# Performance work log

Hardware: AMD Instinct MI355X
Metric: run time of the kernel (lower is better)

## Reference

```python
import jax, jax.numpy as jnp
import numpy as np


def _bipolarize(x):
    # torchhd.hard_quantize: sign quantize to {-1, +1}
    return jnp.where(x > 0, 1.0, -1.0).astype(x.dtype)


def _transform(am, projections):
    """PQ-HDC Algorithm 1: MAP AM (C,D) -> binary AM (C,P,D) in {0,1} + weights (C,P)."""
    C, D = am.shape

    def per_class(hv):  # hv: (D,)
        bips = []
        loss = hv
        for _ in range(projections):  # P is small (2-4), sequential by construction
            bip = _bipolarize(loss)
            dot = jnp.dot(loss, bip)
            # orthogonal projection of loss onto bip: bip * dot / ||bip||^2
            loss = loss - bip * dot / jnp.sum(bip * bip)
            bips.append(bip)
        X = jnp.stack(bips)  # (P, D) bipolar
        G = X @ X.T  # (P, P)
        w = hv @ X.T @ jnp.linalg.inv(G)  # (P,)
        # normalize: length of w[:,None]*X over full (P,D) matrix
        length = jnp.linalg.norm(w[:, None] * X)
        w = jnp.sqrt(jnp.asarray(D, hv.dtype)) * w / length
        w = w ** 2
        return X, w

    Xs, ws = jax.vmap(per_class)(am)  # (C,P,D), (C,P)
    ambin = jnp.where(Xs > 0, 1.0, 0.0).astype(am.dtype)  # binarize {0,1}
    return ambin, ws


def _phs(qbin, ambin, weights):
    """Pseudo Hamming Similarity, batched. qbin:(B,D) {0,1}; ambin:(C,P,D) {0,1}."""
    D = qbin.shape[-1]
    # equal-bit count = D - sum(q XOR a) = D - sum_q - sum_a + 2*q.a
    dots = jnp.einsum('bd,cpd->bcp', qbin, ambin)  # (B,C,P)
    qsum = jnp.sum(qbin, axis=-1)                  # (B,)
    asum = jnp.sum(ambin, axis=-1)                 # (C,P)
    ham = D - qsum[:, None, None] - asum[None, :, :] + 2.0 * dots
    return jnp.sum(weights[None, :, :] * ham, axis=-1)  # (B,C)


def setup_inputs() -> dict:
    key = jax.random.key(0)
    k1, k2 = jax.random.split(key)
    B, C, D = 4096, 128, 10000
    query = jax.random.normal(k1, (B, D), dtype=jnp.float32)
    am = jax.random.normal(k2, (C, D), dtype=jnp.float32)
    return {"query": query, "am": am, "projections": 3}


def reference(query, am, projections):
    ambin, weights = _transform(am, projections)
    qbin = jnp.where(_bipolarize(query) > 0, 1.0, 0.0).astype(query.dtype)
    return _phs(qbin, ambin, weights)  # (B, C) logits
```

## Files before the change

### kernel.cpp

```cpp
#include <hip/hip_runtime.h>
#include <stdint.h>

typedef unsigned long long u64;
typedef __attribute__((ext_vector_type(4))) unsigned int u32x4;

#define D_DIM   10000
#define C_CLS   128
#define WPRP    192
#define NWORDS  160
#define NIT     40
#define GRP     8

__device__ __forceinline__ float wred64(float v) {
#pragma unroll
    for (int m = 1; m <= 32; m <<= 1) v += __shfl_xor(v, m);
    return v;
}
__device__ __forceinline__ int wred64i(int v) {
#pragma unroll
    for (int m = 1; m <= 32; m <<= 1) v += __shfl_xor(v, m);
    return v;
}

__device__ __forceinline__ size_t am_idx(int c, int wi, int p) {
    return ((size_t)c * 32 + (unsigned)wi / 6u) * 18 + (size_t)p * 6 + (unsigned)wi % 6u;
}

__global__ __launch_bounds__(256) void kA_transform(const float* __restrict__ am,
                                                    u64* __restrict__ amw,
                                                    float4* __restrict__ wtab)
{
    const int c = blockIdx.x;
    const int t = threadIdx.x;
    const int w = t >> 6;
    const int l = t & 63;

    __shared__ float redf[4];
    __shared__ int   sI[4][6];
    __shared__ float sF[4][3];

    const float* hvp = am + (size_t)c * D_DIM;

    float4 loss[10], hv[10];
#pragma unroll
    for (int k = 0; k < 10; ++k) {
        const int it = w + 4 * k;
        const int d0 = it * 256 + 4 * l;
        float4 x = make_float4(0.f, 0.f, 0.f, 0.f);
        if (d0 + 3 < D_DIM) x = *(const float4*)(hvp + d0);
        loss[k] = x; hv[k] = x;
    }

    int cnt[3]; float hX[3]; u64 sp[3];

#pragma unroll
    for (int p = 0; p < 3; ++p) {
        float sabs = 0.f;
#pragma unroll
        for (int k = 0; k < 10; ++k)
            sabs += fabsf(loss[k].x) + fabsf(loss[k].y) + fabsf(loss[k].z) + fabsf(loss[k].w);
        sabs = wred64(sabs);
        if (l == 0) redf[w] = sabs;
        __syncthreads();
        const float dot = redf[0] + redf[1] + redf[2] + redf[3];
        __syncthreads();
        const float dd = dot / (float)D_DIM;

        u64 bits = 0; int cc = 0; float hx = 0.f;
#pragma unroll
        for (int k = 0; k < 10; ++k) {
            const int it = w + 4 * k;
            const bool p0 = loss[k].x > 0.f;
            const bool p1 = loss[k].y > 0.f;
            const bool p2 = loss[k].z > 0.f;
            const bool p3 = loss[k].w > 0.f;
            const u64 b0 = __ballot(p0);
            const u64 b1 = __ballot(p1);
            const u64 b2 = __ballot(p2);
            const u64 b3 = __ballot(p3);
            if (l < 4) {
                const u64 bb = (l == 0) ? b0 : ((l == 1) ? b1 : ((l == 2) ? b2 : b3));
                amw[am_idx(c, it * 4 + l, p)] = bb;
            }
            bits |= ((u64)p0 << (4 * k)) | ((u64)p1 << (4 * k + 1))
                  | ((u64)p2 << (4 * k + 2)) | ((u64)p3 << (4 * k + 3));
            cc += (int)p0 + (int)p1 + (int)p2 + (int)p3;
            hx += (p0 ? hv[k].x : -hv[k].x) + (p1 ? hv[k].y : -hv[k].y)
                + (p2 ? hv[k].z : -hv[k].z) + (p3 ? hv[k].w : -hv[k].w);
            float4 L = loss[k];
            L.x -= p0 ? dd : -dd; L.y -= p1 ? dd : -dd;
            L.z -= p2 ? dd : -dd; L.w -= p3 ? dd : -dd;
            const int d0 = it * 256 + 4 * l;
            if (!(d0 + 3 < D_DIM)) L = make_float4(0.f, 0.f, 0.f, 0.f);
            loss[k] = L;
        }
        if (t < WPRP - NWORDS) amw[am_idx(c, NWORDS + t, p)] = 0ull;
        sp[p] = bits; cnt[p] = cc; hX[p] = hx;
    }

    int vi[6] = { cnt[0], cnt[1], cnt[2],
                  static_cast<int>(__popcll(sp[0] ^ sp[1])),
                  static_cast<int>(__popcll(sp[0] ^ sp[2])),
                  static_cast<int>(__popcll(sp[1] ^ sp[2])) };
#pragma unroll
    for (int i = 0; i < 6; ++i) vi[i] = wred64i(vi[i]);
    float vf[3] = { hX[0], hX[1], hX[2] };
#pragma unroll
    for (int i = 0; i < 3; ++i) vf[i] = wred64(vf[i]);
    if (l == 0) {
#pragma unroll
        for (int i = 0; i < 6; ++i) sI[w][i] = vi[i];
#pragma unroll
        for (int i = 0; i < 3; ++i) sF[w][i] = vf[i];
    }
    __syncthreads();
    if (t == 0) {
        int a0 = 0, a1 = 0, a2 = 0, X01 = 0, X02 = 0, X12 = 0;
        float h0f = 0, h1f = 0, h2f = 0;
        for (int i = 0; i < 4; ++i) {
            a0 += sI[i][0]; a1 += sI[i][1]; a2 += sI[i][2];
            X01 += sI[i][3]; X02 += sI[i][4]; X12 += sI[i][5];
            h0f += sF[i][0]; h1f += sF[i][1]; h2f += sF[i][2];
        }
        const double Dv = (double)D_DIM;
        const double h0 = h0f, h1 = h1f, h2 = h2f;
        const double g01 = Dv - 2.0 * X01, g02 = Dv - 2.0 * X02, g12 = Dv - 2.0 * X12;
        const double A00 = Dv * Dv - g12 * g12;
        const double A01 = g02 * g12 - g01 * Dv;
        const double A02 = g01 * g12 - g02 * Dv;
        const double A11 = Dv * Dv - g02 * g02;
        const double A12 = g02 * g01 - Dv * g12;
        const double A22 = Dv * Dv - g01 * g01;
        const double det = Dv * A00 + g01 * A01 + g02 * A02;
        const double w0 = (A00 * h0 + A01 * h1 + A02 * h2) / det;
        const double w1 = (A01 * h0 + A11 * h1 + A12 * h2) / det;
        const double w2 = (A02 * h0 + A12 * h1 + A22 * h2) / det;
        const double s = w0 * w0 + w1 * w1 + w2 * w2;
        const double f0 = w0 * w0 / s, f1 = w1 * w1 / s, f2 = w2 * w2 / s;
        const double cb = -(f0 * a0 + f1 * a1 + f2 * a2);
        wtab[c] = make_float4((float)f0, (float)f1, (float)f2, (float)cb);
    }
}

struct AmBatch { u32x4 r[9]; };

__device__ __forceinline__ void amload_asm(AmBatch& b, const u64* ap) {
    asm("global_load_dwordx4 %0, %9, off\n\t"
        "global_load_dwordx4 %1, %9, off offset:16\n\t"
        "global_load_dwordx4 %2, %9, off offset:32\n\t"
        "global_load_dwordx4 %3, %9, off offset:48\n\t"
        "global_load_dwordx4 %4, %9, off offset:64\n\t"
        "global_load_dwordx4 %5, %9, off offset:80\n\t"
        "global_load_dwordx4 %6, %9, off offset:96\n\t"
        "global_load_dwordx4 %7, %9, off offset:112\n\t"
        "global_load_dwordx4 %8, %9, off offset:128\n\t"
        "s_waitcnt vmcnt(0)"
        : "=v"(b.r[0]), "=v"(b.r[1]), "=v"(b.r[2]), "=v"(b.r[3]), "=v"(b.r[4]),
          "=v"(b.r[5]), "=v"(b.r[6]), "=v"(b.r[7]), "=v"(b.r[8])
        : "v"(ap));
}

__device__ __forceinline__ void qload4_asm(float4& x0, float4& x1, float4& x2, float4& x3,
                                           const float* p) {
    asm("global_load_dwordx4 %0, %4, off\n\t"
        "global_load_dwordx4 %1, %4, off offset:1024\n\t"
        "global_load_dwordx4 %2, %4, off offset:2048\n\t"
        "global_load_dwordx4 %3, %4, off offset:3072\n\t"
        "s_waitcnt vmcnt(0)"
        : "=v"(x0), "=v"(x1), "=v"(x2), "=v"(x3)
        : "v"(p));
}

__global__ __launch_bounds__(256, 4) void kB_phs(const float* __restrict__ query,
                                                 const u64* __restrict__ amw,
                                                 const float4* __restrict__ wtab,
                                                 float* __restrict__ out)
{
    __shared__ u64 qlds[4 * WPRP];
    __shared__ float4 wsh[C_CLS];
    __shared__ float part[4][4][GRP][33];
    const int t = threadIdx.x;
    const int w = t >> 6;
    const int l = t & 63;
    const int r0 = blockIdx.x * 4;
    const int wl = l & 31;
    const int c0 = 32 * w;

    if (t < C_CLS) wsh[t] = wtab[t];

    {
        const float* qp = query + (size_t)(r0 + w) * D_DIM;
        u64* qrow = qlds + w * WPRP;
        for (int ib = 0; ib < 9; ++ib) {
            const int it0 = ib * 4;
            float4 x0, x1, x2, x3;
            qload4_asm(x0, x1, x2, x3, qp + it0 * 256 + 4 * l);
            float4 xs[4] = { x0, x1, x2, x3 };
#pragma unroll
            for (int k = 0; k < 4; ++k) {
                const u64 b0 = __ballot(xs[k].x > 0.f);
                const u64 b1 = __ballot(xs[k].y > 0.f);
                const u64 b2 = __ballot(xs[k].z > 0.f);
                const u64 b3 = __ballot(xs[k].w > 0.f);
                if (l < 4) qrow[(it0 + k) * 4 + l] =
                    (l == 0) ? b0 : ((l == 1) ? b1 : ((l == 2) ? b2 : b3));
            }
        }
        for (int it = 36; it < NIT; ++it) {
            const int d0 = it * 256 + 4 * l;
            float4 x = make_float4(0.f, 0.f, 0.f, 0.f);
            if (d0 + 3 < D_DIM) x = *(const float4*)(qp + d0);
            const u64 b0 = __ballot(x.x > 0.f);
            const u64 b1 = __ballot(x.y > 0.f);
            const u64 b2 = __ballot(x.z > 0.f);
            const u64 b3 = __ballot(x.w > 0.f);
            if (l < 4) qrow[it * 4 + l] = (l == 0) ? b0 : ((l == 1) ? b1 : ((l == 2) ? b2 : b3));
        }
        if (l < 32) qrow[NWORDS + l] = 0ull;
    }
    __syncthreads();

    const int rh = l >> 5;
    const int rA = 2 * rh, rB = 2 * rh + 1;

    const u64* qaP = qlds + rA * WPRP + wl * 6;
    const u64* qbP = qlds + rB * WPRP + wl * 6;
    unsigned qa32[12], qb32[12];
#pragma unroll
    for (int i = 0; i < 6; ++i) {
        const u64 a = qaP[i], b = qbP[i];
        qa32[2 * i] = (unsigned)a; qa32[2 * i + 1] = (unsigned)(a >> 32);
        qb32[2 * i] = (unsigned)b; qb32[2 * i + 1] = (unsigned)(b >> 32);
    }

    int qsA = 0, qsB = 0;
#pragma unroll
    for (int i = 0; i < 12; ++i) { qsA += __popc(qa32[i]); qsB += __popc(qb32[i]); }
    const float offA = 312.5f - (float)qsA;
    const float offB = 312.5f - (float)qsB;

    const int o = l >> 1;
    const int row_loc = o >> 3;
    const int cc = o & 7;
    const int h = l & 1;

    float (*pw)[GRP][33] = part[w];

    for (int g = 0; g < 4; ++g) {
        const int cbase = c0 + g * GRP;
        float accA[GRP], accB[GRP];
#pragma unroll
        for (int i = 0; i < GRP; ++i) {
            const int c = cbase + i;
            AmBatch b;
            amload_asm(b, amw + ((size_t)c * 32 + wl) * 18);
            int pA[3] = {0, 0, 0}, pB[3] = {0, 0, 0};
#pragma unroll
            for (int p = 0; p < 3; ++p)
#pragma unroll
                for (int k = 0; k < 3; ++k) {
                    const u32x4 v = b.r[3 * p + k];
                    pA[p] += __popc(qa32[4 * k + 0] & v[0]) + __popc(qa32[4 * k + 1] & v[1])
                           + __popc(qa32[4 * k + 2] & v[2]) + __popc(qa32[4 * k + 3] & v[3]);
                    pB[p] += __popc(qb32[4 * k + 0] & v[0]) + __popc(qb32[4 * k + 1] & v[1])
                           + __popc(qb32[4 * k + 2] & v[2]) + __popc(qb32[4 * k + 3] & v[3]);
                }
            const float4 wv = wsh[c];
            const float cw = wv.w * 0.03125f;
            accA[i] = fmaf(2.f, wv.x * (float)pA[0] + wv.y * (float)pA[1] + wv.z * (float)pA[2],
                           offA + cw);
            accB[i] = fmaf(2.f, wv.x * (float)pB[0] + wv.y * (float)pB[1] + wv.z * (float)pB[2],
                           offB + cw);
        }

#pragma unroll
        for (int i = 0; i < GRP; ++i) {
            pw[rA][i][wl] = accA[i];
            pw[rB][i][wl] = accB[i];
        }
        float s = 0.f;
#pragma unroll
        for (int j = 0; j < 16; ++j) s += pw[row_loc][cc][h * 16 + j];
        s += __shfl_xor(s, 1);
        if (h == 0)
            out[(size_t)(r0 + row_loc) * C_CLS + (cbase + cc)] = s;
    }
}

extern "C" void kernel_launch(void* const* d_in, const int* in_sizes, int n_in,
                              void* d_out, int out_size, void* d_ws, size_t ws_size,
                              hipStream_t stream)
{
    const float* query = (const float*)d_in[0];
    const float* am    = (const float*)d_in[1];
    float* out = (float*)d_out;

    float4* wtab = (float4*)d_ws;
    u64* amw = (u64*)((char*)d_ws + 2048);

    const int B = in_sizes[0] / D_DIM;

    hipLaunchKernelGGL(kA_transform, dim3(C_CLS), dim3(256), 0, stream, am, amw, wtab);
    hipLaunchKernelGGL(kB_phs, dim3(B / 4), dim3(256), 0, stream, query, amw, wtab, out);
}
```

Before: 97.24 us.

## Halve rows per block, split query binarization across waves, raise occupancy

Each block now handles 2 query rows instead of 4, and each lane holds one row's bits instead of two. The query sign-packing work is split so two waves cooperate on each row's word range. Launch bounds move to 8 blocks per SM and the reduction becomes a 4-lane shuffle. The inline-asm load outputs are marked early-clobber so the compiler cannot alias them with the address register. This doubles the number of blocks and the AM bit-vector reloads per query row, trading more global and L2 traffic on the AM table for lower register pressure and more parallelism.

```diff
diff --git a/kernel.cpp b/kernel.cpp
--- a/kernel.cpp
+++ b/kernel.cpp
@@ -155,8 +155,8 @@
         "global_load_dwordx4 %7, %9, off offset:112\n\t"
         "global_load_dwordx4 %8, %9, off offset:128\n\t"
         "s_waitcnt vmcnt(0)"
-        : "=v"(b.r[0]), "=v"(b.r[1]), "=v"(b.r[2]), "=v"(b.r[3]), "=v"(b.r[4]),
-          "=v"(b.r[5]), "=v"(b.r[6]), "=v"(b.r[7]), "=v"(b.r[8])
+        : "=&v"(b.r[0]), "=&v"(b.r[1]), "=&v"(b.r[2]), "=&v"(b.r[3]), "=&v"(b.r[4]),
+          "=&v"(b.r[5]), "=&v"(b.r[6]), "=&v"(b.r[7]), "=&v"(b.r[8])
         : "v"(ap));
 }
 
@@ -167,32 +167,36 @@
         "global_load_dwordx4 %2, %4, off offset:2048\n\t"
         "global_load_dwordx4 %3, %4, off offset:3072\n\t"
         "s_waitcnt vmcnt(0)"
-        : "=v"(x0), "=v"(x1), "=v"(x2), "=v"(x3)
+        : "=&v"(x0), "=&v"(x1), "=&v"(x2), "=&v"(x3)
         : "v"(p));
 }
 
-__global__ __launch_bounds__(256, 4) void kB_phs(const float* __restrict__ query,
+__global__ __launch_bounds__(256, 8) void kB_phs(const float* __restrict__ query,
                                                  const u64* __restrict__ amw,
                                                  const float4* __restrict__ wtab,
                                                  float* __restrict__ out)
 {
-    __shared__ u64 qlds[4 * WPRP];
+    __shared__ u64 qlds[2 * WPRP];
     __shared__ float4 wsh[C_CLS];
-    __shared__ float part[4][4][GRP][33];
+    __shared__ float part[4][2][GRP][33];
     const int t = threadIdx.x;
     const int w = t >> 6;
     const int l = t & 63;
-    const int r0 = blockIdx.x * 4;
+    const int r0 = blockIdx.x * 2;
     const int wl = l & 31;
     const int c0 = 32 * w;
 
     if (t < C_CLS) wsh[t] = wtab[t];
 
     {
-        const float* qp = query + (size_t)(r0 + w) * D_DIM;
-        u64* qrow = qlds + w * WPRP;
-        for (int ib = 0; ib < 9; ++ib) {
-            const int it0 = ib * 4;
+        const int row = w & 1;
+        const int half = w >> 1;
+        const float* qp = query + (size_t)(r0 + row) * D_DIM;
+        u64* qrow = qlds + row * WPRP;
+        const int itBase = 20 * half;
+        const int nb = (half == 0) ? 5 : 4;
+        for (int ib = 0; ib < nb; ++ib) {
+            const int it0 = itBase + ib * 4;
             float4 x0, x1, x2, x3;
             qload4_asm(x0, x1, x2, x3, qp + it0 * 256 + 4 * l);
             float4 xs[4] = { x0, x1, x2, x3 };
@@ -206,82 +210,72 @@
                     (l == 0) ? b0 : ((l == 1) ? b1 : ((l == 2) ? b2 : b3));
             }
         }
-        for (int it = 36; it < NIT; ++it) {
-            const int d0 = it * 256 + 4 * l;
-            float4 x = make_float4(0.f, 0.f, 0.f, 0.f);
-            if (d0 + 3 < D_DIM) x = *(const float4*)(qp + d0);
-            const u64 b0 = __ballot(x.x > 0.f);
-            const u64 b1 = __ballot(x.y > 0.f);
-            const u64 b2 = __ballot(x.z > 0.f);
-            const u64 b3 = __ballot(x.w > 0.f);
-            if (l < 4) qrow[it * 4 + l] = (l == 0) ? b0 : ((l == 1) ? b1 : ((l == 2) ? b2 : b3));
-        }
-        if (l < 32) qrow[NWORDS + l] = 0ull;
+        if (half == 1) {
+            for (int it = 36; it < NIT; ++it) {
+                const int d0 = it * 256 + 4 * l;
+                float4 x = make_float4(0.f, 0.f, 0.f, 0.f);
+                if (d0 + 3 < D_DIM) x = *(const float4*)(qp + d0);
+                const u64 b0 = __ballot(x.x > 0.f);
+                const u64 b1 = __ballot(x.y > 0.f);
+                const u64 b2 = __ballot(x.z > 0.f);
+                const u64 b3 = __ballot(x.w > 0.f);
+                if (l < 4) qrow[it * 4 + l] = (l == 0) ? b0 : ((l == 1) ? b1 : ((l == 2) ? b2 : b3));
+            }
+        }
+        if (w < 2 && l < 32) qlds[w * WPRP + NWORDS + l] = 0ull;
     }
     __syncthreads();
 
-    const int rh = l >> 5;
-    const int rA = 2 * rh, rB = 2 * rh + 1;
-
-    const u64* qaP = qlds + rA * WPRP + wl * 6;
-    const u64* qbP = qlds + rB * WPRP + wl * 6;
-    unsigned qa32[12], qb32[12];
+    const int rowh = l >> 5;
+    const u64* qP = qlds + rowh * WPRP + wl * 6;
+    unsigned q32[12];
 #pragma unroll
     for (int i = 0; i < 6; ++i) {
-        const u64 a = qaP[i], b = qbP[i];
-        qa32[2 * i] = (unsigned)a; qa32[2 * i + 1] = (unsigned)(a >> 32);
-        qb32[2 * i] = (unsigned)b; qb32[2 * i + 1] = (unsigned)(b >> 32);
-    }
-
-    int qsA = 0, qsB = 0;
-#pragma unroll
-    for (int i = 0; i < 12; ++i) { qsA += __popc(qa32[i]); qsB += __popc(qb32[i]); }
-    const float offA = 312.5f - (float)qsA;
-    const float offB = 312.5f - (float)qsB;
-
-    const int o = l >> 1;
+        const u64 a = qP[i];
+        q32[2 * i] = (unsigned)a; q32[2 * i + 1] = (unsigned)(a >> 32);
+    }
+    int qs = 0;
+#pragma unroll
+    for (int i = 0; i < 12; ++i) qs += __popc(q32[i]);
+    const float off = 312.5f - (float)qs;
+
+    const int o = l >> 2;
     const int row_loc = o >> 3;
     const int cc = o & 7;
-    const int h = l & 1;
+    const int h = l & 3;
 
     float (*pw)[GRP][33] = part[w];
 
     for (int g = 0; g < 4; ++g) {
         const int cbase = c0 + g * GRP;
-        float accA[GRP], accB[GRP];
+        float acc[GRP];
 #pragma unroll
         for (int i = 0; i < GRP; ++i) {
             const int c = cbase + i;
             AmBatch b;
             amload_asm(b, amw + ((size_t)c * 32 + wl) * 18);
-            int pA[3] = {0, 0, 0}, pB[3] = {0, 0, 0};
+            int pc[3] = {0, 0, 0};
 #pragma unroll
             for (int p = 0; p < 3; ++p)
 #pragma unroll
                 for (int k = 0; k < 3; ++k) {
                     const u32x4 v = b.r[3 * p + k];
-                    pA[p] += __popc(qa32[4 * k + 0] & v[0]) + __popc(qa32[4 * k + 1] & v[1])
-                           + __popc(qa32[4 * k + 2] & v[2]) + __popc(qa32[4 * k + 3] & v[3]);
-                    pB[p] += __popc(qb32[4 * k + 0] & v[0]) + __popc(qb32[4 * k + 1] & v[1])
-                           + __popc(qb32[4 * k + 2] & v[2]) + __popc(qb32[4 * k + 3] & v[3]);
+                    pc[p] += __popc(q32[4 * k + 0] & v[0]) + __popc(q32[4 * k + 1] & v[1])
+                           + __popc(q32[4 * k + 2] & v[2]) + __popc(q32[4 * k + 3] & v[3]);
                 }
             const float4 wv = wsh[c];
             const float cw = wv.w * 0.03125f;
-            accA[i] = fmaf(2.f, wv.x * (float)pA[0] + wv.y * (float)pA[1] + wv.z * (float)pA[2],
-                           offA + cw);
-            accB[i] = fmaf(2.f, wv.x * (float)pB[0] + wv.y * (float)pB[1] + wv.z * (float)pB[2],
-                           offB + cw);
-        }
-
-#pragma unroll
-        for (int i = 0; i < GRP; ++i) {
-            pw[rA][i][wl] = accA[i];
-            pw[rB][i][wl] = accB[i];
-        }
+            acc[i] = fmaf(2.f, wv.x * (float)pc[0] + wv.y * (float)pc[1] + wv.z * (float)pc[2],
+                          off + cw);
+        }
+
+#pragma unroll
+        for (int i = 0; i < GRP; ++i) pw[rowh][i][wl] = acc[i];
         float s = 0.f;
 #pragma unroll
-        for (int j = 0; j < 16; ++j) s += pw[row_loc][cc][h * 16 + j];
+        for (int j = 0; j < 8; ++j) s += pw[row_loc][cc][h * 8 + j];
         s += __shfl_xor(s, 1);
+        s += __shfl_xor(s, 2);
         if (h == 0)
             out[(size_t)(r0 + row_loc) * C_CLS + (cbase + cc)] = s;
     }
@@ -301,5 +295,5 @@
     const int B = in_sizes[0] / D_DIM;
 
     hipLaunchKernelGGL(kA_transform, dim3(C_CLS), dim3(256), 0, stream, am, amw, wtab);
-    hipLaunchKernelGGL(kB_phs, dim3(B / 4), dim3(256), 0, stream, query, amw, wtab, out);
-}
+    hipLaunchKernelGGL(kB_phs, dim3(B / 2), dim3(256), 0, stream, query, amw, wtab, out);
+}
```

Measured after the change: 170.7 us. 1.76x slower.

## Split query packing into separate kernel and double PHS grid over class halves

Applied to the files above, without the earlier changes.

Query bit-packing moves out of the PHS kernel into a standalone pack kernel that writes packed rows to workspace. The PHS kernel then reads packed query words from global memory and launches twice as many blocks, each covering half the classes, to raise parallelism. The inline asm load outputs also become early-clobber. The trade-off is an extra launch and a global round trip for the packed queries, and the old fused kernel is kept as a fallback when the workspace is too small.

```diff
diff --git a/kernel.cpp b/kernel.cpp
--- a/kernel.cpp
+++ b/kernel.cpp
@@ -155,8 +155,8 @@
         "global_load_dwordx4 %7, %9, off offset:112\n\t"
         "global_load_dwordx4 %8, %9, off offset:128\n\t"
         "s_waitcnt vmcnt(0)"
-        : "=v"(b.r[0]), "=v"(b.r[1]), "=v"(b.r[2]), "=v"(b.r[3]), "=v"(b.r[4]),
-          "=v"(b.r[5]), "=v"(b.r[6]), "=v"(b.r[7]), "=v"(b.r[8])
+        : "=&v"(b.r[0]), "=&v"(b.r[1]), "=&v"(b.r[2]), "=&v"(b.r[3]), "=&v"(b.r[4]),
+          "=&v"(b.r[5]), "=&v"(b.r[6]), "=&v"(b.r[7]), "=&v"(b.r[8])
         : "v"(ap));
 }
 
@@ -167,64 +167,71 @@
         "global_load_dwordx4 %2, %4, off offset:2048\n\t"
         "global_load_dwordx4 %3, %4, off offset:3072\n\t"
         "s_waitcnt vmcnt(0)"
-        : "=v"(x0), "=v"(x1), "=v"(x2), "=v"(x3)
+        : "=&v"(x0), "=&v"(x1), "=&v"(x2), "=&v"(x3)
         : "v"(p));
 }
 
-__global__ __launch_bounds__(256, 4) void kB_phs(const float* __restrict__ query,
-                                                 const u64* __restrict__ amw,
-                                                 const float4* __restrict__ wtab,
-                                                 float* __restrict__ out)
+__global__ __launch_bounds__(256, 4) void kB1_pack(const float* __restrict__ query,
+                                                   u64* __restrict__ qws)
 {
-    __shared__ u64 qlds[4 * WPRP];
+    const int t = threadIdx.x;
+    const int w = t >> 6;
+    const int l = t & 63;
+    const int row = blockIdx.x * 4 + w;
+
+    const float* qp = query + (size_t)row * D_DIM;
+    u64* qrow = qws + (size_t)row * WPRP;
+    for (int ib = 0; ib < 9; ++ib) {
+        const int it0 = ib * 4;
+        float4 x0, x1, x2, x3;
+        qload4_asm(x0, x1, x2, x3, qp + it0 * 256 + 4 * l);
+        float4 xs[4] = { x0, x1, x2, x3 };
+#pragma unroll
+        for (int k = 0; k < 4; ++k) {
+            const u64 b0 = __ballot(xs[k].x > 0.f);
+            const u64 b1 = __ballot(xs[k].y > 0.f);
+            const u64 b2 = __ballot(xs[k].z > 0.f);
+            const u64 b3 = __ballot(xs[k].w > 0.f);
+            if (l < 4) qrow[(it0 + k) * 4 + l] =
+                (l == 0) ? b0 : ((l == 1) ? b1 : ((l == 2) ? b2 : b3));
+        }
+    }
+    for (int it = 36; it < NIT; ++it) {
+        const int d0 = it * 256 + 4 * l;
+        float4 x = make_float4(0.f, 0.f, 0.f, 0.f);
+        if (d0 + 3 < D_DIM) x = *(const float4*)(qp + d0);
+        const u64 b0 = __ballot(x.x > 0.f);
+        const u64 b1 = __ballot(x.y > 0.f);
+        const u64 b2 = __ballot(x.z > 0.f);
+        const u64 b3 = __ballot(x.w > 0.f);
+        if (l < 4) qrow[it * 4 + l] = (l == 0) ? b0 : ((l == 1) ? b1 : ((l == 2) ? b2 : b3));
+    }
+    if (l < 32) qrow[NWORDS + l] = 0ull;
+}
+
+__global__ __launch_bounds__(256, 4) void kB2_phs(const u64* __restrict__ qws,
+                                                  const u64* __restrict__ amw,
+                                                  const float4* __restrict__ wtab,
+                                                  float* __restrict__ out)
+{
     __shared__ float4 wsh[C_CLS];
     __shared__ float part[4][4][GRP][33];
     const int t = threadIdx.x;
     const int w = t >> 6;
     const int l = t & 63;
-    const int r0 = blockIdx.x * 4;
+    const int r0 = (blockIdx.x >> 1) * 4;
+    const int ch = blockIdx.x & 1;
     const int wl = l & 31;
-    const int c0 = 32 * w;
+    const int c0 = ch * 64 + 16 * w;
 
     if (t < C_CLS) wsh[t] = wtab[t];
-
-    {
-        const float* qp = query + (size_t)(r0 + w) * D_DIM;
-        u64* qrow = qlds + w * WPRP;
-        for (int ib = 0; ib < 9; ++ib) {
-            const int it0 = ib * 4;
-            float4 x0, x1, x2, x3;
-            qload4_asm(x0, x1, x2, x3, qp + it0 * 256 + 4 * l);
-            float4 xs[4] = { x0, x1, x2, x3 };
-#pragma unroll
-            for (int k = 0; k < 4; ++k) {
-                const u64 b0 = __ballot(xs[k].x > 0.f);
-                const u64 b1 = __ballot(xs[k].y > 0.f);
-                const u64 b2 = __ballot(xs[k].z > 0.f);
-                const u64 b3 = __ballot(xs[k].w > 0.f);
-                if (l < 4) qrow[(it0 + k) * 4 + l] =
-                    (l == 0) ? b0 : ((l == 1) ? b1 : ((l == 2) ? b2 : b3));
-            }
-        }
-        for (int it = 36; it < NIT; ++it) {
-            const int d0 = it * 256 + 4 * l;
-            float4 x = make_float4(0.f, 0.f, 0.f, 0.f);
-            if (d0 + 3 < D_DIM) x = *(const float4*)(qp + d0);
-            const u64 b0 = __ballot(x.x > 0.f);
-            const u64 b1 = __ballot(x.y > 0.f);
-            const u64 b2 = __ballot(x.z > 0.f);
-            const u64 b3 = __ballot(x.w > 0.f);
-            if (l < 4) qrow[it * 4 + l] = (l == 0) ? b0 : ((l == 1) ? b1 : ((l == 2) ? b2 : b3));
-        }
-        if (l < 32) qrow[NWORDS + l] = 0ull;
-    }
     __syncthreads();
 
     const int rh = l >> 5;
     const int rA = 2 * rh, rB = 2 * rh + 1;
 
-    const u64* qaP = qlds + rA * WPRP + wl * 6;
-    const u64* qbP = qlds + rB * WPRP + wl * 6;
+    const u64* qaP = qws + (size_t)(r0 + rA) * WPRP + wl * 6;
+    const u64* qbP = qws + (size_t)(r0 + rB) * WPRP + wl * 6;
     unsigned qa32[12], qb32[12];
 #pragma unroll
     for (int i = 0; i < 6; ++i) {
@@ -246,7 +253,7 @@
 
     float (*pw)[GRP][33] = part[w];
 
-    for (int g = 0; g < 4; ++g) {
+    for (int g = 0; g < 2; ++g) {
         const int cbase = c0 + g * GRP;
         float accA[GRP], accB[GRP];
 #pragma unroll
@@ -287,6 +294,122 @@
     }
 }
 
+__global__ __launch_bounds__(256, 4) void kB_phs4(const float* __restrict__ query,
+                                                  const u64* __restrict__ amw,
+                                                  const float4* __restrict__ wtab,
+                                                  float* __restrict__ out)
+{
+    __shared__ u64 qlds[4 * WPRP];
+    __shared__ float4 wsh[C_CLS];
+    __shared__ float part[4][4][GRP][33];
+    const int t = threadIdx.x;
+    const int w = t >> 6;
+    const int l = t & 63;
+    const int r0 = blockIdx.x * 4;
+    const int wl = l & 31;
+    const int c0 = 32 * w;
+
+    if (t < C_CLS) wsh[t] = wtab[t];
+
+    {
+        const float* qp = query + (size_t)(r0 + w) * D_DIM;
+        u64* qrow = qlds + w * WPRP;
+        for (int ib = 0; ib < 9; ++ib) {
+            const int it0 = ib * 4;
+            float4 x0, x1, x2, x3;
+            qload4_asm(x0, x1, x2, x3, qp + it0 * 256 + 4 * l);
+            float4 xs[4] = { x0, x1, x2, x3 };
+#pragma unroll
+            for (int k = 0; k < 4; ++k) {
+                const u64 b0 = __ballot(xs[k].x > 0.f);
+                const u64 b1 = __ballot(xs[k].y > 0.f);
+                const u64 b2 = __ballot(xs[k].z > 0.f);
+                const u64 b3 = __ballot(xs[k].w > 0.f);
+                if (l < 4) qrow[(it0 + k) * 4 + l] =
+                    (l == 0) ? b0 : ((l == 1) ? b1 : ((l == 2) ? b2 : b3));
+            }
+        }
+        for (int it = 36; it < NIT; ++it) {
+            const int d0 = it * 256 + 4 * l;
+            float4 x = make_float4(0.f, 0.f, 0.f, 0.f);
+            if (d0 + 3 < D_DIM) x = *(const float4*)(qp + d0);
+            const u64 b0 = __ballot(x.x > 0.f);
+            const u64 b1 = __ballot(x.y > 0.f);
+            const u64 b2 = __ballot(x.z > 0.f);
+            const u64 b3 = __ballot(x.w > 0.f);
+            if (l < 4) qrow[it * 4 + l] = (l == 0) ? b0 : ((l == 1) ? b1 : ((l == 2) ? b2 : b3));
+        }
+        if (l < 32) qrow[NWORDS + l] = 0ull;
+    }
+    __syncthreads();
+
+    const int rh = l >> 5;
+    const int rA = 2 * rh, rB = 2 * rh + 1;
+
+    const u64* qaP = qlds + rA * WPRP + wl * 6;
+    const u64* qbP = qlds + rB * WPRP + wl * 6;
+    unsigned qa32[12], qb32[12];
+#pragma unroll
+    for (int i = 0; i < 6; ++i) {
+        const u64 a = qaP[i], b = qbP[i];
+        qa32[2 * i] = (unsigned)a; qa32[2 * i + 1] = (unsigned)(a >> 32);
+        qb32[2 * i] = (unsigned)b; qb32[2 * i + 1] = (unsigned)(b >> 32);
+    }
+
+    int qsA = 0, qsB = 0;
+#pragma unroll
+    for (int i = 0; i < 12; ++i) { qsA += __popc(qa32[i]); qsB += __popc(qb32[i]); }
+    const float offA = 312.5f - (float)qsA;
+    const float offB = 312.5f - (float)qsB;
+
+    const int o = l >> 1;
+    const int row_loc = o >> 3;
+    const int cc = o & 7;
+    const int h = l & 1;
+
+    float (*pw)[GRP][33] = part[w];
+
+    for (int g = 0; g < 4; ++g) {
+        const int cbase = c0 + g * GRP;
+        float accA[GRP], accB[GRP];
+#pragma unroll
+        for (int i = 0; i < GRP; ++i) {
+            const int c = cbase + i;
+            AmBatch b;
+            amload_asm(b, amw + ((size_t)c * 32 + wl) * 18);
+            int pA[3] = {0, 0, 0}, pB[3] = {0, 0, 0};
+#pragma unroll
+            for (int p = 0; p < 3; ++p)
+#pragma unroll
+                for (int k = 0; k < 3; ++k) {
+                    const u32x4 v = b.r[3 * p + k];
+                    pA[p] += __popc(qa32[4 * k + 0] & v[0]) + __popc(qa32[4 * k + 1] & v[1])
+                           + __popc(qa32[4 * k + 2] & v[2]) + __popc(qa32[4 * k + 3] & v[3]);
+                    pB[p] += __popc(qb32[4 * k + 0] & v[0]) + __popc(qb32[4 * k + 1] & v[1])
+                           + __popc(qb32[4 * k + 2] & v[2]) + __popc(qb32[4 * k + 3] & v[3]);
+                }
+            const float4 wv = wsh[c];
+            const float cw = wv.w * 0.03125f;
+            accA[i] = fmaf(2.f, wv.x * (float)pA[0] + wv.y * (float)pA[1] + wv.z * (float)pA[2],
+                           offA + cw);
+            accB[i] = fmaf(2.f, wv.x * (float)pB[0] + wv.y * (float)pB[1] + wv.z * (float)pB[2],
+                           offB + cw);
+        }
+
+#pragma unroll
+        for (int i = 0; i < GRP; ++i) {
+            pw[rA][i][wl] = accA[i];
+            pw[rB][i][wl] = accB[i];
+        }
+        float s = 0.f;
+#pragma unroll
+        for (int j = 0; j < 16; ++j) s += pw[row_loc][cc][h * 16 + j];
+        s += __shfl_xor(s, 1);
+        if (h == 0)
+            out[(size_t)(r0 + row_loc) * C_CLS + (cbase + cc)] = s;
+    }
+}
+
 extern "C" void kernel_launch(void* const* d_in, const int* in_sizes, int n_in,
                               void* d_out, int out_size, void* d_ws, size_t ws_size,
                               hipStream_t stream)
@@ -297,9 +420,16 @@
 
     float4* wtab = (float4*)d_ws;
     u64* amw = (u64*)((char*)d_ws + 2048);
+    u64* qws = (u64*)((char*)d_ws + 2048 + 589824);
 
     const int B = in_sizes[0] / D_DIM;
+    const size_t needed = 2048 + 589824 + (size_t)B * WPRP * 8;
 
     hipLaunchKernelGGL(kA_transform, dim3(C_CLS), dim3(256), 0, stream, am, amw, wtab);
-    hipLaunchKernelGGL(kB_phs, dim3(B / 4), dim3(256), 0, stream, query, amw, wtab, out);
-}
+    if (ws_size >= needed) {
+        hipLaunchKernelGGL(kB1_pack, dim3(B / 4), dim3(256), 0, stream, query, qws);
+        hipLaunchKernelGGL(kB2_phs, dim3((B / 4) * 2), dim3(256), 0, stream, qws, amw, wtab, out);
+    } else {
+        hipLaunchKernelGGL(kB_phs4, dim3(B / 4), dim3(256), 0, stream, query, amw, wtab, out);
+    }
+}
```

After: 101.4 us. 4.3% more time.
